# Kernel optimization log

Measured on AMD Instinct MI355X. Metric: run time of the kernel, lower is better.

Reference implementation:

```python
import math
import jax, jax.numpy as jnp
import numpy as np

B, C, H, W = 8, 256, 32, 32
NH, DK, DV = 8, 32, 32
EPS = 1e-6


def mish(x):
    return x * jnp.tanh(jax.nn.softplus(x))


def grouped_conv1x1(x, w, b, groups):
    # x: (B, Cin, N); w: (Cout, Cin//groups); b: (Cout,)
    Bb, Cin, N = x.shape
    Cout = w.shape[0]
    xg = x.reshape(Bb, groups, Cin // groups, N)
    wg = w.reshape(groups, Cout // groups, Cin // groups)
    y = jnp.einsum('bgin,goi->bgon', xg, wg).reshape(Bb, Cout, N)
    return y + b[None, :, None]


def conv_block(x, w, b, s, beta, groups):
    # 1x1 conv -> BatchNorm (eval: running mean 0 / var 1 => affine) -> Mish
    y = grouped_conv1x1(x, w, b, groups)
    y = s[None, :, None] * y + beta[None, :, None]
    return mish(y)


def setup_inputs() -> dict:
    key = jax.random.key(0)
    ks = jax.random.split(key, 8)
    inp = {
        'x': jax.random.normal(ks[0], (B, C, H, W), dtype=jnp.float32),
        'q_w': jax.random.normal(ks[1], (NH * DK, C // NH), dtype=jnp.float32) * 0.05,
        'q_b': jnp.zeros((NH * DK,), jnp.float32),
        'q_s': jnp.ones((NH * DK,), jnp.float32),
        'q_beta': jnp.zeros((NH * DK,), jnp.float32),
        'k_w': jax.random.normal(ks[2], (NH * DK, C // NH), dtype=jnp.float32) * 0.05,
        'k_b': jnp.zeros((NH * DK,), jnp.float32),
        'k_s': jnp.ones((NH * DK,), jnp.float32),
        'k_beta': jnp.zeros((NH * DK,), jnp.float32),
        'v_w': jax.random.normal(ks[3], (NH * DV, C // NH), dtype=jnp.float32) * 0.05,
        'v_b': jnp.zeros((NH * DV,), jnp.float32),
        'v_s': jnp.ones((NH * DV,), jnp.float32),
        'v_beta': jnp.zeros((NH * DV,), jnp.float32),
        'f_w': jax.random.normal(ks[4], (C, NH * DV), dtype=jnp.float32) * 0.05,
        'f_b': jnp.zeros((C,), jnp.float32),
        'f_s': jnp.ones((C,), jnp.float32),
        'f_beta': jnp.zeros((C,), jnp.float32),
    }
    return inp


def _forward(x, q_w, q_b, q_s, q_beta, k_w, k_b, k_s, k_beta,
             v_w, v_b, v_s, v_beta, f_w, f_b, f_s, f_beta):
    b, c, h, w = x.shape
    n = h * w
    temp = math.sqrt(c / NH)
    xf = x.reshape(b, c, n)

    q = conv_block(xf, q_w, q_b, q_s, q_beta, NH).reshape(b, NH, DK, n) / temp
    k = conv_block(xf, k_w, k_b, k_s, k_beta, NH).reshape(b, NH, DK, n)
    v = conv_block(xf, v_w, v_b, v_s, v_beta, NH).reshape(b, NH, DV, n)

    # cosine-distance attention (all heads vectorized); identical math to the
    # torch broadcast/repeat version but computed via normalized dot products.
    qn = jnp.sqrt(jnp.sum(q * q, axis=2))  # (b, nh, n)
    kn = jnp.sqrt(jnp.sum(k * k, axis=2))
    dot = jnp.einsum('bhdn,bhdm->bhnm', q, k)  # (b, nh, n, n)
    denom = jnp.maximum(qn[:, :, :, None] * kn[:, :, None, :], EPS)
    cos = jnp.clip(dot / denom, -1.0 + 1e-6, 1.0 - 1e-6)
    attn = jax.nn.softmax(1.0 - jnp.arccos(cos) / math.pi, axis=-1)

    # out[..., d, i] = sum_m v[..., d, m] * attn[..., i, m]
    out = jnp.einsum('bhdm,bhnm->bhdn', v, attn).reshape(b, NH * DV, n)

    y = conv_block(out, f_w, f_b, f_s, f_beta, 1).reshape(b, c, h, w) + x

    # extract_attn_map (no_grad in original)
    am = jnp.sum(jnp.mean(attn, axis=1), axis=1)  # (b, n)
    mn = jnp.min(am, axis=1, keepdims=True)
    mx = jnp.max(am, axis=1, keepdims=True)
    am = ((am - mn) / (mx - mn)).reshape(b, h, w)
    return y, jax.lax.stop_gradient(am)


def reference(x, q_w, q_b, q_s, q_beta, k_w, k_b, k_s, k_beta,
              v_w, v_b, v_s, v_beta, f_w, f_b, f_s, f_beta):
    return _forward(x, q_w, q_b, q_s, q_beta, k_w, k_b, k_s, k_beta,
                    v_w, v_b, v_s, v_beta, f_w, f_b, f_s, f_beta)
```

## Files before the change

kernel.cpp:

```cpp
#include <hip/hip_runtime.h>
#include <math.h>

#define B_   8
#define C_   256
#define NH_  8
#define N_   1024
#define LOG2E    1.4426950408889634f

typedef __attribute__((ext_vector_type(8))) short bf16x8;
typedef __attribute__((ext_vector_type(4))) float f32x4;
typedef __attribute__((ext_vector_type(2))) float f32x2;
typedef unsigned short u16;
typedef unsigned int u32;

#define AS1 __attribute__((address_space(1)))
#define AS3 __attribute__((address_space(3)))

__device__ __forceinline__ f32x4 mfma16(bf16x8 a, bf16x8 b, f32x4 c) {
    return __builtin_amdgcn_mfma_f32_16x16x32_bf16(a, b, c, 0, 0, 0);
}
__device__ __forceinline__ u32 bf16r(float x) {
    u32 b = __float_as_uint(x);
    return (b + 0x7fffu + ((b >> 16) & 1u)) >> 16;
}
__device__ __forceinline__ float mish_fast(float x) {
    float e  = __builtin_amdgcn_exp2f(fminf(x, 30.f) * LOG2E);
    float nm = e * (e + 2.f);
    return x * nm * __builtin_amdgcn_rcpf(nm + 2.f);
}
__device__ __forceinline__ f32x2 splat2(float v) { return (f32x2){v, v}; }
__device__ __forceinline__ f32x2 fexp_poly2(f32x2 c) {
    c = __builtin_elementwise_min(
            __builtin_elementwise_max(c, splat2(-0.999999f)), splat2(0.999999f));
    f32x2 u = c * c;
    f32x2 p = __builtin_elementwise_fma(splat2(1.7809920f), u, splat2(-3.7571968f));
    f32x2 q = __builtin_elementwise_fma(splat2(6.3713280f), u, splat2(-15.1427584f));
    p = __builtin_elementwise_fma(p, u, splat2(2.8140000f));
    q = __builtin_elementwise_fma(q, u, splat2(13.1518784f));
    p = __builtin_elementwise_fma(p, u, splat2(-0.8122592f));
    q = __builtin_elementwise_fma(q, u, splat2(-4.8903712f));
    p = __builtin_elementwise_fma(p, u, splat2(0.1705120f));
    q = __builtin_elementwise_fma(q, u, splat2(0.8441120f));
    p = __builtin_elementwise_fma(p, u, splat2(1.6473155f));
    q = __builtin_elementwise_fma(q, u, splat2(0.4936541f));
    return __builtin_elementwise_fma(c, q, p);
}

__global__ __launch_bounds__(256) void qkvpack_kernel(
    const float* __restrict__ x,
    const float* __restrict__ qw, const float* __restrict__ qb2,
    const float* __restrict__ qs, const float* __restrict__ qbeta,
    const float* __restrict__ kw, const float* __restrict__ kb2,
    const float* __restrict__ ks, const float* __restrict__ kbeta,
    const float* __restrict__ vw, const float* __restrict__ vb2,
    const float* __restrict__ vs, const float* __restrict__ vbeta,
    uint4* __restrict__ qpk, uint4* __restrict__ kpk, u16* __restrict__ vbf,
    const float* __restrict__ fw, u16* __restrict__ wbf)
{
    int blk = blockIdx.x;
    if (blk >= 768) {
        int id = (blk - 768) * 1024 + threadIdx.x;
#pragma unroll
        for (int j = 0; j < 4; ++j) { int p = id + j * 256; wbf[p] = (u16)bf16r(fw[p]); }
        return;
    }
    int type = blk >> 8;
    int sub = blk & 255;
    int nt = sub & 3, g = (sub >> 2) & 7, b = sub >> 5;
    int n = nt * 256 + threadIdx.x;
    int bh = b * 8 + g;
    const float* xp = x + ((size_t)b * C_ + g * 32) * N_ + n;
    float xv[32];
#pragma unroll
    for (int i = 0; i < 32; ++i) xv[i] = xp[(size_t)i * N_];

    const float *w, *bb, *sc, *bt;
    if (type == 0)      { w = qw; bb = qb2; sc = qs; bt = qbeta; }
    else if (type == 1) { w = kw; bb = kb2; sc = ks; bt = kbeta; }
    else                { w = vw; bb = vb2; sc = vs; bt = vbeta; }

    float y[32];
#pragma unroll
    for (int co = 0; co < 32; ++co) {
        int cg = g * 32 + co;
        float acc = 0.f;
#pragma unroll
        for (int i = 0; i < 32; ++i)
            acc = fmaf(xv[i], w[cg * 32 + i], acc);
        y[co] = mish_fast(sc[cg] * (acc + bb[cg]) + bt[cg]);
    }

    if (type == 2) {
#pragma unroll
        for (int co = 0; co < 32; ++co)
            vbf[((size_t)bh * 32 + co) * N_ + n] = (u16)bf16r(y[co]);
        return;
    }
    float s2 = 0.f;
#pragma unroll
    for (int d = 0; d < 32; ++d) s2 = fmaf(y[d], y[d], s2);
    float inv = __builtin_amdgcn_rsqf(fmaxf(s2, 1e-24f));
    u32 wp[16];
#pragma unroll
    for (int d = 0; d < 16; ++d)
        wp[d] = bf16r(y[2 * d] * inv) | (bf16r(y[2 * d + 1] * inv) << 16);
    uint4* dst = (type == 0 ? qpk : kpk) + ((size_t)bh * N_ + n) * 4;
#pragma unroll
    for (int j = 0; j < 4; ++j)
        dst[j] = make_uint4(wp[4 * j], wp[4 * j + 1], wp[4 * j + 2], wp[4 * j + 3]);
}

__global__ __launch_bounds__(256) void attn_kernel(
    const u16* __restrict__ qpk, const u16* __restrict__ kpk,
    const u16* __restrict__ vbf,
    u16* __restrict__ aout_bt, float* __restrict__ ampart)
{
    __shared__ __align__(16) u16 KV[512 * 8];
    __shared__ __align__(16) u16 Ps[4][16 * 136];
    __shared__ __align__(16) float amW[N_];

    const int tid  = threadIdx.x;
    const int wave = tid >> 6, lane = tid & 63;
    const int l15 = lane & 15, lg = lane >> 4;
    const int swz = (blockIdx.x & 7) * 128 + (blockIdx.x >> 3);
    const int itile = swz & 15, bh = swz >> 4;
    const int h = bh & 7, bidx = bh >> 3;
    const int i0 = itile * 64;

    const char* ksrc = (const char*)(kpk + (size_t)bh * N_ * 32);
    const char* vsrc = (const char*)(vbf + (size_t)bh * 32 * N_);
    const char* qsrc = (const char*)(qpk + (size_t)bh * N_ * 32);

    for (int j = tid; j < N_; j += 256) amW[j] = 0.f;

    const int kj0 = tid >> 7, km0g = tid & 127;
    const int kj1 = (256 + tid) >> 7, km1g = (256 + tid) & 127;
    const int vd0 = tid >> 4, vg0 = tid & 15;
    const int vd1 = (256 + tid) >> 4, vg1 = (256 + tid) & 15;
    const size_t koff0 = (size_t)km0g * 64 + kj0 * 16;
    const size_t koff1 = (size_t)km1g * 64 + kj1 * 16;
    const size_t voff0 = (size_t)vd0 * 2048 + ((vg0 ^ (vd0 & 7)) << 4);
    const size_t voff1 = (size_t)vd1 * 2048 + ((vg1 ^ (vd1 & 7)) << 4);

    bf16x8 aq = *(const bf16x8*)(qsrc + (size_t)(i0 + wave * 16 + l15) * 64 + lg * 16);

    const char* kfb = (const char*)KV + lg * 2048 + l15 * 16;

    u32 fc[128];

    uint4 kreg0 = *(const uint4*)(ksrc + koff0);
    uint4 kreg1 = *(const uint4*)(ksrc + koff1);
    f32x2 rsL = {0.f, 0.f}, rsH = {0.f, 0.f};
#pragma unroll
    for (int ch = 0; ch < 8; ++ch) {
        *(uint4*)((char*)KV + tid * 16)         = kreg0;
        *(uint4*)((char*)KV + (256 + tid) * 16) = kreg1;
        if (ch < 7) {
            kreg0 = *(const uint4*)(ksrc + (size_t)(ch + 1) * 8192 + koff0);
            kreg1 = *(const uint4*)(ksrc + (size_t)(ch + 1) * 8192 + koff1);
        }
        asm volatile("s_waitcnt lgkmcnt(0)" ::: "memory");
        __builtin_amdgcn_sched_barrier(0);
        __builtin_amdgcn_s_barrier();
        __builtin_amdgcn_sched_barrier(0);
#pragma unroll
        for (int t = 0; t < 8; ++t) {
            bf16x8 bk = *(const bf16x8*)(kfb + t * 256);
            f32x4 cf = {0.f, 0.f, 0.f, 0.f};
            cf = mfma16(aq, bk, cf);
            f32x2 fL = fexp_poly2((f32x2){cf[0], cf[1]});
            f32x2 fH = fexp_poly2((f32x2){cf[2], cf[3]});
            rsL += fL; rsH += fH;
            fc[ch * 16 + t * 2]     = bf16r(fL.x) | (bf16r(fL.y) << 16);
            fc[ch * 16 + t * 2 + 1] = bf16r(fH.x) | (bf16r(fH.y) << 16);
        }
        asm volatile("s_waitcnt lgkmcnt(0)" ::: "memory");
        __builtin_amdgcn_sched_barrier(0);
        __builtin_amdgcn_s_barrier();
        __builtin_amdgcn_sched_barrier(0);
    }
    float rinv[4];
    {
        float rr[4] = {rsL.x, rsL.y, rsH.x, rsH.y};
#pragma unroll
        for (int r = 0; r < 4; ++r) {
            float s = rr[r];
            s += __shfl_xor(s, 1); s += __shfl_xor(s, 2);
            s += __shfl_xor(s, 4); s += __shfl_xor(s, 8);
            rinv[r] = __builtin_amdgcn_rcpf(s);
        }
    }
    f32x2 rinvL = {rinv[0], rinv[1]}, rinvH = {rinv[2], rinv[3]};

    f32x4 o0 = {0.f, 0.f, 0.f, 0.f}, o1 = {0.f, 0.f, 0.f, 0.f};
    char*       psw = (char*)&Ps[wave][0] + lg * 1088 + l15 * 2;
    const char* pab = (const char*)&Ps[wave][0] + l15 * 272 + lg * 16;
    const char* vfb = (const char*)KV + l15 * 256;
    const int   vkey = l15 & 7;

    uint4 vreg0 = *(const uint4*)(vsrc + voff0);
    uint4 vreg1 = *(const uint4*)(vsrc + voff1);

#pragma unroll
    for (int ch = 0; ch < 8; ++ch) {
        *(uint4*)((char*)KV + tid * 16)         = vreg0;
        *(uint4*)((char*)KV + (256 + tid) * 16) = vreg1;
        if (ch < 7) {
            vreg0 = *(const uint4*)(vsrc + (size_t)(ch + 1) * 256 + voff0);
            vreg1 = *(const uint4*)(vsrc + (size_t)(ch + 1) * 256 + voff1);
        }
        asm volatile("s_waitcnt lgkmcnt(0)" ::: "memory");
        __builtin_amdgcn_sched_barrier(0);
        __builtin_amdgcn_s_barrier();
        __builtin_amdgcn_sched_barrier(0);

#pragma unroll
        for (int t = 0; t < 8; ++t) {
            u32 r0 = fc[ch * 16 + t * 2];
            u32 r1 = fc[ch * 16 + t * 2 + 1];
            *(u16*)(psw + 0 * 272 + t * 32) = (u16)r0;
            *(u16*)(psw + 1 * 272 + t * 32) = (u16)(r0 >> 16);
            *(u16*)(psw + 2 * 272 + t * 32) = (u16)r1;
            *(u16*)(psw + 3 * 272 + t * 32) = (u16)(r1 >> 16);
            f32x2 fL = {__uint_as_float(r0 << 16), __uint_as_float(r0 & 0xffff0000u)};
            f32x2 fH = {__uint_as_float(r1 << 16), __uint_as_float(r1 & 0xffff0000u)};
            f32x2 cs2 = fL * rinvL;
            cs2 = __builtin_elementwise_fma(fH, rinvH, cs2);
            float csum = cs2.x + cs2.y;
            csum += __shfl_xor(csum, 16);
            csum += __shfl_xor(csum, 32);
            if (lane < 16) atomicAdd(&amW[ch * 128 + t * 16 + l15], csum);
        }
        asm volatile("s_waitcnt lgkmcnt(0)" ::: "memory");
        __builtin_amdgcn_sched_barrier(0);
#pragma unroll
        for (int kss = 0; kss < 4; ++kss) {
            bf16x8 pa = *(const bf16x8*)(pab + kss * 64);
            const char* va = vfb + (((kss * 4 + lg) ^ vkey) << 4);
            bf16x8 v0 = *(const bf16x8*)va;
            bf16x8 v1 = *(const bf16x8*)(va + 4096);
            o0 = mfma16(pa, v0, o0);
            o1 = mfma16(pa, v1, o1);
        }
        asm volatile("s_waitcnt lgkmcnt(0)" ::: "memory");
        __builtin_amdgcn_sched_barrier(0);
        __builtin_amdgcn_s_barrier();
        __builtin_amdgcn_sched_barrier(0);
    }
    __syncthreads();

    {
        u16* oT = (u16*)Ps;
#pragma unroll
        for (int r = 0; r < 4; ++r) {
            int irow = wave * 16 + lg * 4 + r;
            oT[irow * 40 + l15]      = (u16)bf16r(o0[r] * rinv[r]);
            oT[irow * 40 + 16 + l15] = (u16)bf16r(o1[r] * rinv[r]);
        }
    }
    __syncthreads();
    {
        const u16* oT = (const u16*)Ps;
        int row = tid >> 2, c4 = tid & 3;
        uint4 val = *(const uint4*)((const char*)oT + row * 80 + c4 * 16);
        int n = i0 + row;
        int g = h * 4 + c4;
        size_t dst = ((size_t)(bidx * N_ + n) << 9) + ((size_t)((g ^ (row & 7)) << 4));
        *(uint4*)((char*)aout_bt + dst) = val;
    }
#pragma unroll
    for (int j2 = 0; j2 < 4; ++j2)
        ampart[(size_t)swz * N_ + tid + 256 * j2] = amW[tid + 256 * j2];
}

__global__ __launch_bounds__(256) void fconv_kernel(
    const u16* __restrict__ aout_bt, const u16* __restrict__ wbf,
    const float* __restrict__ x,
    const float* __restrict__ fs, const float* __restrict__ fb,
    const float* __restrict__ fbeta, float* __restrict__ y,
    const float* __restrict__ ampart, float* __restrict__ outAm)
{
    __shared__ __align__(16) u16 As[32 * 256];
    __shared__ float rmn[256], rmx[256];
    const int tid = threadIdx.x;

    if (blockIdx.x >= 256) {
        int b = blockIdx.x - 256;
        const float* base = ampart + (size_t)b * 128 * N_;
        float s[4] = {0.f, 0.f, 0.f, 0.f};
        for (int p = 0; p < 128; ++p) {
#pragma unroll
            for (int c2 = 0; c2 < 4; ++c2)
                s[c2] += base[(size_t)p * N_ + tid + 256 * c2];
        }
        float mn = fminf(fminf(s[0], s[1]), fminf(s[2], s[3]));
        float mx = fmaxf(fmaxf(s[0], s[1]), fmaxf(s[2], s[3]));
        rmn[tid] = mn; rmx[tid] = mx;
        __syncthreads();
        for (int off = 128; off >= 1; off >>= 1) {
            if (tid < off) {
                rmn[tid] = fminf(rmn[tid], rmn[tid + off]);
                rmx[tid] = fmaxf(rmx[tid], rmx[tid + off]);
            }
            __syncthreads();
        }
        mn = rmn[0]; mx = rmx[0];
        float inv = 1.f / (mx - mn);
#pragma unroll
        for (int c2 = 0; c2 < 4; ++c2)
            outAm[(size_t)b * N_ + tid + 256 * c2] = (s[c2] - mn) * inv;
        return;
    }

    const int wave = tid >> 6, lane = tid & 63;
    const int l15 = lane & 15, lg = lane >> 4;
    const int b  = blockIdx.x >> 5;
    const int n0 = (blockIdx.x & 31) * 32;

    const char* asrc = (const char*)aout_bt + ((size_t)(b * N_ + n0) << 9);
#pragma unroll
    for (int p = 0; p < 4; ++p) {
        int g = p * 256 + wave * 64 + lane;
        __builtin_amdgcn_global_load_lds(
            (const AS1 void*)(asrc + g * 16),
            (AS3 void*)((char*)As + ((p * 256 + wave * 64) << 4)), 16, 0, 0);
    }
    __syncthreads();

    f32x4 acc[4][2];
#pragma unroll
    for (int f = 0; f < 4; ++f)
#pragma unroll
        for (int fn = 0; fn < 2; ++fn) acc[f][fn] = (f32x4){0.f, 0.f, 0.f, 0.f};

    const int cobase = wave * 64;
#pragma unroll
    for (int kk = 0; kk < 8; ++kk) {
        bf16x8 af[2];
#pragma unroll
        for (int fn = 0; fn < 2; ++fn) {
            int nf = fn * 16 + l15;
            af[fn] = *(const bf16x8*)((const char*)As + nf * 512 +
                                      (((kk * 4 + lg) ^ (nf & 7)) << 4));
        }
#pragma unroll
        for (int f = 0; f < 4; ++f) {
            bf16x8 wf = *(const bf16x8*)(wbf + (size_t)(cobase + f * 16 + l15) * 256 + kk * 32 + lg * 8);
            acc[f][0] = mfma16(wf, af[0], acc[f][0]);
            acc[f][1] = mfma16(wf, af[1], acc[f][1]);
        }
    }

#pragma unroll
    for (int f = 0; f < 4; ++f) {
#pragma unroll
        for (int r = 0; r < 4; ++r) {
            int co = cobase + f * 16 + lg * 4 + r;
            float sc = fs[co], bb = fb[co], bt = fbeta[co];
#pragma unroll
            for (int fn = 0; fn < 2; ++fn) {
                int n = n0 + fn * 16 + l15;
                size_t oid = ((size_t)(b * C_ + co) << 10) + n;
                y[oid] = mish_fast(sc * (acc[f][fn][r] + bb) + bt) + x[oid];
            }
        }
    }
}

extern "C" void kernel_launch(void* const* d_in, const int* in_sizes, int n_in,
                              void* d_out, int out_size, void* d_ws, size_t ws_size,
                              hipStream_t stream)
{
    const float* x     = (const float*)d_in[0];
    const float* q_w   = (const float*)d_in[1];
    const float* q_b   = (const float*)d_in[2];
    const float* q_s   = (const float*)d_in[3];
    const float* q_be  = (const float*)d_in[4];
    const float* k_w   = (const float*)d_in[5];
    const float* k_b   = (const float*)d_in[6];
    const float* k_s   = (const float*)d_in[7];
    const float* k_be  = (const float*)d_in[8];
    const float* v_w   = (const float*)d_in[9];
    const float* v_b   = (const float*)d_in[10];
    const float* v_s   = (const float*)d_in[11];
    const float* v_be  = (const float*)d_in[12];
    const float* f_w   = (const float*)d_in[13];
    const float* f_b   = (const float*)d_in[14];
    const float* f_s   = (const float*)d_in[15];
    const float* f_be  = (const float*)d_in[16];

    float* y_out  = (float*)d_out;
    float* am_out = (float*)d_out + (size_t)B_ * C_ * N_;

    char* w = (char*)d_ws;
    u16*   qpk     = (u16*)w;    w += (size_t)B_ * NH_ * N_ * 64;
    u16*   kpk     = (u16*)w;    w += (size_t)B_ * NH_ * N_ * 64;
    u16*   vbf     = (u16*)w;    w += (size_t)B_ * C_ * N_ * 2;
    u16*   aout_bt = (u16*)w;    w += (size_t)B_ * N_ * C_ * 2;
    float* ampart  = (float*)w;  w += (size_t)B_ * NH_ * 16 * N_ * 4;
    u16*   wbf     = (u16*)w;

    qkvpack_kernel<<<832, 256, 0, stream>>>(
        x, q_w, q_b, q_s, q_be, k_w, k_b, k_s, k_be,
        v_w, v_b, v_s, v_be, (uint4*)qpk, (uint4*)kpk, vbf, f_w, wbf);

    attn_kernel<<<B_ * NH_ * 16, 256, 0, stream>>>(
        qpk, kpk, vbf, aout_bt, ampart);

    fconv_kernel<<<264, 256, 0, stream>>>(
        aout_bt, wbf, x, f_s, f_b, f_be, y_out, ampart, am_out);
}
```

Measured before the change: 128.9 us.

## Split attention key range across two wave halves and fuse QK with PV

The attention kernel now launches 512 threads per block, and each half of the waves handles half of the key/value range for the same 64 query rows. The separate K pass and V pass are merged into one loop: unnormalized probabilities are written to LDS and multiplied by V immediately, with row sums and partial outputs combined across the halves through shared memory at the end. This halves the per-wave serial loop length and the fc register array, which should allow more waves in flight and fewer barrier rounds. In exchange it uses more LDS, adds a cross-half reduction with extra syncs, and normalizes only after accumulation.

Result: faster. 114.1 us (-11.4%).

```diff
diff --git a/kernel.cpp b/kernel.cpp
--- a/kernel.cpp
+++ b/kernel.cpp
@@ -110,18 +110,22 @@
         dst[j] = make_uint4(wp[4 * j], wp[4 * j + 1], wp[4 * j + 2], wp[4 * j + 3]);
 }
 
-__global__ __launch_bounds__(256) void attn_kernel(
+__global__ __launch_bounds__(512, 4) void attn_kernel(
     const u16* __restrict__ qpk, const u16* __restrict__ kpk,
     const u16* __restrict__ vbf,
     u16* __restrict__ aout_bt, float* __restrict__ ampart)
 {
-    __shared__ __align__(16) u16 KV[512 * 8];
-    __shared__ __align__(16) u16 Ps[4][16 * 136];
+    __shared__ __align__(16) u16 Kl[1024 * 8];
+    __shared__ __align__(16) u16 Vl[1024 * 8];
+    __shared__ __align__(16) u16 Ps[8][16 * 136];
     __shared__ __align__(16) float amW[N_];
+    __shared__ __align__(16) float rsX[8][16];
 
     const int tid  = threadIdx.x;
     const int wave = tid >> 6, lane = tid & 63;
     const int l15 = lane & 15, lg = lane >> 4;
+    const int half = wave >> 2;
+    const int w3 = wave & 3;
     const int swz = (blockIdx.x & 7) * 128 + (blockIdx.x >> 3);
     const int itile = swz & 15, bh = swz >> 4;
     const int h = bh & 7, bidx = bh >> 3;
@@ -131,38 +135,48 @@
     const char* vsrc = (const char*)(vbf + (size_t)bh * 32 * N_);
     const char* qsrc = (const char*)(qpk + (size_t)bh * N_ * 32);
 
-    for (int j = tid; j < N_; j += 256) amW[j] = 0.f;
-
-    const int kj0 = tid >> 7, km0g = tid & 127;
-    const int kj1 = (256 + tid) >> 7, km1g = (256 + tid) & 127;
-    const int vd0 = tid >> 4, vg0 = tid & 15;
-    const int vd1 = (256 + tid) >> 4, vg1 = (256 + tid) & 15;
-    const size_t koff0 = (size_t)km0g * 64 + kj0 * 16;
-    const size_t koff1 = (size_t)km1g * 64 + kj1 * 16;
-    const size_t voff0 = (size_t)vd0 * 2048 + ((vg0 ^ (vd0 & 7)) << 4);
-    const size_t voff1 = (size_t)vd1 * 2048 + ((vg1 ^ (vd1 & 7)) << 4);
-
-    bf16x8 aq = *(const bf16x8*)(qsrc + (size_t)(i0 + wave * 16 + l15) * 64 + lg * 16);
-
-    const char* kfb = (const char*)KV + lg * 2048 + l15 * 16;
-
-    u32 fc[128];
-
-    uint4 kreg0 = *(const uint4*)(ksrc + koff0);
-    uint4 kreg1 = *(const uint4*)(ksrc + koff1);
+    amW[tid] = 0.f; amW[512 + tid] = 0.f;
+
+    const size_t koffL = (size_t)(tid & 127) * 64 + (size_t)(tid >> 7) * 16;
+    const size_t koffH = koffL + 512 * 64;
+    const int vd = tid >> 4, vg = tid & 15;
+    const size_t voffL = (size_t)vd * 2048 + (size_t)((vg ^ (vd & 7)) << 4);
+    const size_t voffH = voffL + 1024;
+
+    bf16x8 aq = *(const bf16x8*)(qsrc + (size_t)(i0 + w3 * 16 + l15) * 64 + lg * 16);
+
+    const char* kfb = (const char*)Kl + half * 8192 + lg * 2048 + l15 * 16;
+    const char* vfb = (const char*)Vl + half * 8192 + l15 * 256;
+    const int   vkey = l15 & 7;
+    char*       psw = (char*)&Ps[wave][0] + lg * 1088 + l15 * 2;
+    const char* pab = (const char*)&Ps[wave][0] + l15 * 272 + lg * 16;
+
+    u32 fc[64];
     f32x2 rsL = {0.f, 0.f}, rsH = {0.f, 0.f};
-#pragma unroll
-    for (int ch = 0; ch < 8; ++ch) {
-        *(uint4*)((char*)KV + tid * 16)         = kreg0;
-        *(uint4*)((char*)KV + (256 + tid) * 16) = kreg1;
-        if (ch < 7) {
-            kreg0 = *(const uint4*)(ksrc + (size_t)(ch + 1) * 8192 + koff0);
-            kreg1 = *(const uint4*)(ksrc + (size_t)(ch + 1) * 8192 + koff1);
+    f32x4 o0 = {0.f, 0.f, 0.f, 0.f}, o1 = {0.f, 0.f, 0.f, 0.f};
+
+    uint4 kregL = *(const uint4*)(ksrc + koffL);
+    uint4 kregH = *(const uint4*)(ksrc + koffH);
+    uint4 vregL = *(const uint4*)(vsrc + voffL);
+    uint4 vregH = *(const uint4*)(vsrc + voffH);
+
+#pragma unroll
+    for (int ch = 0; ch < 4; ++ch) {
+        *(uint4*)((char*)Kl + tid * 16)         = kregL;
+        *(uint4*)((char*)Kl + (512 + tid) * 16) = kregH;
+        *(uint4*)((char*)Vl + tid * 16)         = vregL;
+        *(uint4*)((char*)Vl + (512 + tid) * 16) = vregH;
+        if (ch < 3) {
+            kregL = *(const uint4*)(ksrc + (size_t)(ch + 1) * 8192 + koffL);
+            kregH = *(const uint4*)(ksrc + (size_t)(ch + 1) * 8192 + koffH);
+            vregL = *(const uint4*)(vsrc + (size_t)(ch + 1) * 256 + voffL);
+            vregH = *(const uint4*)(vsrc + (size_t)(ch + 1) * 256 + voffH);
         }
         asm volatile("s_waitcnt lgkmcnt(0)" ::: "memory");
         __builtin_amdgcn_sched_barrier(0);
         __builtin_amdgcn_s_barrier();
         __builtin_amdgcn_sched_barrier(0);
+
 #pragma unroll
         for (int t = 0; t < 8; ++t) {
             bf16x8 bk = *(const bf16x8*)(kfb + t * 256);
@@ -171,57 +185,58 @@
             f32x2 fL = fexp_poly2((f32x2){cf[0], cf[1]});
             f32x2 fH = fexp_poly2((f32x2){cf[2], cf[3]});
             rsL += fL; rsH += fH;
-            fc[ch * 16 + t * 2]     = bf16r(fL.x) | (bf16r(fL.y) << 16);
-            fc[ch * 16 + t * 2 + 1] = bf16r(fH.x) | (bf16r(fH.y) << 16);
+            u32 r0 = bf16r(fL.x) | (bf16r(fL.y) << 16);
+            u32 r1 = bf16r(fH.x) | (bf16r(fH.y) << 16);
+            fc[ch * 16 + t * 2]     = r0;
+            fc[ch * 16 + t * 2 + 1] = r1;
+            *(u16*)(psw + 0 * 272 + t * 32) = (u16)r0;
+            *(u16*)(psw + 1 * 272 + t * 32) = (u16)(r0 >> 16);
+            *(u16*)(psw + 2 * 272 + t * 32) = (u16)r1;
+            *(u16*)(psw + 3 * 272 + t * 32) = (u16)(r1 >> 16);
+        }
+        asm volatile("s_waitcnt lgkmcnt(0)" ::: "memory");
+        __builtin_amdgcn_sched_barrier(0);
+#pragma unroll
+        for (int kss = 0; kss < 4; ++kss) {
+            bf16x8 pa = *(const bf16x8*)(pab + kss * 64);
+            const char* va = vfb + (((kss * 4 + lg) ^ vkey) << 4);
+            bf16x8 v0 = *(const bf16x8*)va;
+            bf16x8 v1 = *(const bf16x8*)(va + 4096);
+            o0 = mfma16(pa, v0, o0);
+            o1 = mfma16(pa, v1, o1);
         }
         asm volatile("s_waitcnt lgkmcnt(0)" ::: "memory");
         __builtin_amdgcn_sched_barrier(0);
         __builtin_amdgcn_s_barrier();
         __builtin_amdgcn_sched_barrier(0);
     }
+
+    float rr[4] = {rsL.x, rsL.y, rsH.x, rsH.y};
+#pragma unroll
+    for (int r = 0; r < 4; ++r) {
+        float s = rr[r];
+        s += __shfl_xor(s, 1); s += __shfl_xor(s, 2);
+        s += __shfl_xor(s, 4); s += __shfl_xor(s, 8);
+        rr[r] = s;
+    }
+    if (l15 == 0) {
+#pragma unroll
+        for (int r = 0; r < 4; ++r) rsX[wave][lg * 4 + r] = rr[r];
+    }
+    __syncthreads();
     float rinv[4];
-    {
-        float rr[4] = {rsL.x, rsL.y, rsH.x, rsH.y};
-#pragma unroll
-        for (int r = 0; r < 4; ++r) {
-            float s = rr[r];
-            s += __shfl_xor(s, 1); s += __shfl_xor(s, 2);
-            s += __shfl_xor(s, 4); s += __shfl_xor(s, 8);
-            rinv[r] = __builtin_amdgcn_rcpf(s);
-        }
-    }
+#pragma unroll
+    for (int r = 0; r < 4; ++r)
+        rinv[r] = __builtin_amdgcn_rcpf(rr[r] + rsX[wave ^ 4][lg * 4 + r]);
     f32x2 rinvL = {rinv[0], rinv[1]}, rinvH = {rinv[2], rinv[3]};
 
-    f32x4 o0 = {0.f, 0.f, 0.f, 0.f}, o1 = {0.f, 0.f, 0.f, 0.f};
-    char*       psw = (char*)&Ps[wave][0] + lg * 1088 + l15 * 2;
-    const char* pab = (const char*)&Ps[wave][0] + l15 * 272 + lg * 16;
-    const char* vfb = (const char*)KV + l15 * 256;
-    const int   vkey = l15 & 7;
-
-    uint4 vreg0 = *(const uint4*)(vsrc + voff0);
-    uint4 vreg1 = *(const uint4*)(vsrc + voff1);
-
-#pragma unroll
-    for (int ch = 0; ch < 8; ++ch) {
-        *(uint4*)((char*)KV + tid * 16)         = vreg0;
-        *(uint4*)((char*)KV + (256 + tid) * 16) = vreg1;
-        if (ch < 7) {
-            vreg0 = *(const uint4*)(vsrc + (size_t)(ch + 1) * 256 + voff0);
-            vreg1 = *(const uint4*)(vsrc + (size_t)(ch + 1) * 256 + voff1);
-        }
-        asm volatile("s_waitcnt lgkmcnt(0)" ::: "memory");
-        __builtin_amdgcn_sched_barrier(0);
-        __builtin_amdgcn_s_barrier();
-        __builtin_amdgcn_sched_barrier(0);
-
+    const int mbase = half * 512;
+#pragma unroll
+    for (int ch = 0; ch < 4; ++ch) {
 #pragma unroll
         for (int t = 0; t < 8; ++t) {
             u32 r0 = fc[ch * 16 + t * 2];
             u32 r1 = fc[ch * 16 + t * 2 + 1];
-            *(u16*)(psw + 0 * 272 + t * 32) = (u16)r0;
-            *(u16*)(psw + 1 * 272 + t * 32) = (u16)(r0 >> 16);
-            *(u16*)(psw + 2 * 272 + t * 32) = (u16)r1;
-            *(u16*)(psw + 3 * 272 + t * 32) = (u16)(r1 >> 16);
             f32x2 fL = {__uint_as_float(r0 << 16), __uint_as_float(r0 & 0xffff0000u)};
             f32x2 fH = {__uint_as_float(r1 << 16), __uint_as_float(r1 & 0xffff0000u)};
             f32x2 cs2 = fL * rinvL;
@@ -229,38 +244,34 @@
             float csum = cs2.x + cs2.y;
             csum += __shfl_xor(csum, 16);
             csum += __shfl_xor(csum, 32);
-            if (lane < 16) atomicAdd(&amW[ch * 128 + t * 16 + l15], csum);
-        }
-        asm volatile("s_waitcnt lgkmcnt(0)" ::: "memory");
-        __builtin_amdgcn_sched_barrier(0);
-#pragma unroll
-        for (int kss = 0; kss < 4; ++kss) {
-            bf16x8 pa = *(const bf16x8*)(pab + kss * 64);
-            const char* va = vfb + (((kss * 4 + lg) ^ vkey) << 4);
-            bf16x8 v0 = *(const bf16x8*)va;
-            bf16x8 v1 = *(const bf16x8*)(va + 4096);
-            o0 = mfma16(pa, v0, o0);
-            o1 = mfma16(pa, v1, o1);
-        }
-        asm volatile("s_waitcnt lgkmcnt(0)" ::: "memory");
-        __builtin_amdgcn_sched_barrier(0);
-        __builtin_amdgcn_s_barrier();
-        __builtin_amdgcn_sched_barrier(0);
+            if (lane < 16) atomicAdd(&amW[mbase + ch * 128 + t * 16 + l15], csum);
+        }
     }
     __syncthreads();
 
-    {
-        u16* oT = (u16*)Ps;
+    float* Obuf = (float*)Ps;
+    if (half == 1) {
 #pragma unroll
         for (int r = 0; r < 4; ++r) {
-            int irow = wave * 16 + lg * 4 + r;
-            oT[irow * 40 + l15]      = (u16)bf16r(o0[r] * rinv[r]);
-            oT[irow * 40 + 16 + l15] = (u16)bf16r(o1[r] * rinv[r]);
+            int row = w3 * 16 + lg * 4 + r;
+            Obuf[row * 33 + l15]      = o0[r];
+            Obuf[row * 33 + 16 + l15] = o1[r];
         }
     }
     __syncthreads();
-    {
-        const u16* oT = (const u16*)Ps;
+    u16* oT = (u16*)((char*)Ps + 9216);
+    if (half == 0) {
+#pragma unroll
+        for (int r = 0; r < 4; ++r) {
+            int row = w3 * 16 + lg * 4 + r;
+            float a0 = (o0[r] + Obuf[row * 33 + l15])      * rinv[r];
+            float a1 = (o1[r] + Obuf[row * 33 + 16 + l15]) * rinv[r];
+            oT[row * 40 + l15]      = (u16)bf16r(a0);
+            oT[row * 40 + 16 + l15] = (u16)bf16r(a1);
+        }
+    }
+    __syncthreads();
+    if (tid < 256) {
         int row = tid >> 2, c4 = tid & 3;
         uint4 val = *(const uint4*)((const char*)oT + row * 80 + c4 * 16);
         int n = i0 + row;
@@ -268,9 +279,8 @@
         size_t dst = ((size_t)(bidx * N_ + n) << 9) + ((size_t)((g ^ (row & 7)) << 4));
         *(uint4*)((char*)aout_bt + dst) = val;
     }
-#pragma unroll
-    for (int j2 = 0; j2 < 4; ++j2)
-        ampart[(size_t)swz * N_ + tid + 256 * j2] = amW[tid + 256 * j2];
+    ampart[(size_t)swz * N_ + tid]       = amW[tid];
+    ampart[(size_t)swz * N_ + 512 + tid] = amW[512 + tid];
 }
 
 __global__ __launch_bounds__(256) void fconv_kernel(
@@ -404,7 +414,7 @@
         x, q_w, q_b, q_s, q_be, k_w, k_b, k_s, k_be,
         v_w, v_b, v_s, v_be, (uint4*)qpk, (uint4*)kpk, vbf, f_w, wbf);
 
-    attn_kernel<<<B_ * NH_ * 16, 256, 0, stream>>>(
+    attn_kernel<<<B_ * NH_ * 16, 512, 0, stream>>>(
         qpk, kpk, vbf, aout_bt, ampart);
 
     fconv_kernel<<<264, 256, 0, stream>>>(
```
